# Kernel optimization log

Hardware: AMD Instinct MI355X
Metric: run time of the kernel (lower is better)

## Reference

```python
import jax, jax.numpy as jnp
import numpy as np

# model_grid_shape (flipped ensemble grid, all equal here); E = 8 experts
GRID = (2, 2, 2)
E = GRID[0] * GRID[1] * GRID[2]
N = 524288   # query points
H = 64       # sub-model MLP hidden width


def setup_inputs() -> dict:
    key = jax.random.key(0)
    ks = jax.random.split(key, 4)
    # query coordinates in [-1, 1]^3
    x = jax.random.uniform(ks[0], (N, 3), jnp.float32, -1.0, 1.0)
    # per-expert spatial extents: axis-aligned cells tiling [-1,1]^3, in the
    # same flat order as the routing index i0 + i1*g0 + i2*g0*g1
    i = np.arange(E)
    cell = np.stack([i % GRID[0], (i // GRID[0]) % GRID[1],
                     i // (GRID[0] * GRID[1])], axis=-1).astype(np.float32)
    g = np.array(GRID, np.float32)
    extents_min = jnp.asarray(-1.0 + 2.0 * cell / g)          # [E, 3]
    extents_max = jnp.asarray(-1.0 + 2.0 * (cell + 1.0) / g)  # [E, 3]
    # per-expert SRN MLP parameters: 3 -> H -> H -> 1
    W1 = jax.random.normal(ks[1], (E, 3, H), jnp.float32) / np.sqrt(3.0)
    b1 = jnp.zeros((E, H), jnp.float32)
    W2 = jax.random.normal(ks[2], (E, H, H), jnp.float32) / np.sqrt(float(H))
    b2 = jnp.zeros((E, H), jnp.float32)
    W3 = jax.random.normal(ks[3], (E, H, 1), jnp.float32) / np.sqrt(float(H))
    b3 = jnp.zeros((E, 1), jnp.float32)
    return {"x": x, "extents_min": extents_min, "extents_max": extents_max,
            "W1": W1, "b1": b1, "W2": W2, "b2": b2, "W3": W3, "b3": b3}


def reference(x, extents_min, extents_max, W1, b1, W2, b2, W3, b3):
    # --- routing: flat expert index per point (matches torch forward) ---
    u = jnp.clip((x + 1.0) * 0.5, 0.0, 0.99)
    gvec = jnp.asarray(GRID, x.dtype)
    gi = (u * gvec).astype(jnp.int32)                       # [N, 3]
    idx = gi[:, 0] + gi[:, 1] * GRID[0] + gi[:, 2] * (GRID[0] * GRID[1])

    # --- dispatch/combine: scan over experts, masked scatter into y ---
    def body(y, args):
        i, emin, emax, w1, bb1, w2, bb2, w3, bb3 = args
        # normalize point into expert-local [-1, 1]^3
        xn = -1.0 + 2.0 * ((x - emin) / (emax - emin))      # [N, 3]
        h = jax.nn.relu(xn @ w1 + bb1)                      # [N, H]
        h = jax.nn.relu(h @ w2 + bb2)                       # [N, H]
        o = h @ w3 + bb3                                    # [N, 1]
        mask = (idx == i)[:, None]
        return jnp.where(mask, o, y), None

    y0 = jnp.zeros((x.shape[0], 1), x.dtype)
    y, _ = jax.lax.scan(
        body, y0,
        (jnp.arange(E), extents_min, extents_max, W1, b1, W2, b2, W3, b3))
    return y
```

## Files before the change

### kernel.cpp

```cpp
#include <hip/hip_runtime.h>

typedef __bf16 bf16x8 __attribute__((ext_vector_type(8)));
typedef __bf16 bf16x2 __attribute__((ext_vector_type(2)));
typedef float f32x4 __attribute__((ext_vector_type(4)));
typedef float f32x2 __attribute__((ext_vector_type(2)));

#define N_PTS 524288
#define SBLK 256
#define PTS_PER_SBLK 2048
#define CAP 73728

__device__ __forceinline__ unsigned short f2bf(float f) {
    unsigned u = __float_as_uint(f);
    u += 0x7FFFu + ((u >> 16) & 1u);
    return (unsigned short)(u >> 16);
}

__device__ __forceinline__ int route(float x0, float x1, float x2) {
    int g0 = (int)(fminf(fmaxf((x0 + 1.0f) * 0.5f, 0.0f), 0.99f) * 2.0f);
    int g1 = (int)(fminf(fmaxf((x1 + 1.0f) * 0.5f, 0.0f), 0.99f) * 2.0f);
    int g2 = (int)(fminf(fmaxf((x2 + 1.0f) * 0.5f, 0.0f), 0.99f) * 2.0f);
    return g0 + 2*g1 + 4*g2;
}

#define OFF_CNT  0u
#define OFF_XG   1024u

extern "C" __global__ void __launch_bounds__(256) k3_scatter(
        const float* __restrict__ x, int* __restrict__ cursor,
        float4* __restrict__ xg) {
    __shared__ int lh[8];
    __shared__ int startS[8];
    int t = threadIdx.x;
    if (t < 8) lh[t] = 0;
    __syncthreads();
    int base = blockIdx.x * PTS_PER_SBLK;
    float c0[8], c1[8], c2[8];
    unsigned epack = 0;
    #pragma unroll
    for (int i = 0; i < 8; ++i) {
        int p = base + i * 256 + t;
        c0[i] = x[3*p]; c1[i] = x[3*p+1]; c2[i] = x[3*p+2];
        int e = route(c0[i], c1[i], c2[i]);
        epack |= (unsigned)e << (3*i);
        atomicAdd(&lh[e], 1);
    }
    __syncthreads();
    if (t < 8) { startS[t] = atomicAdd(&cursor[t], lh[t]); lh[t] = 0; }
    __syncthreads();
    #pragma unroll
    for (int i = 0; i < 8; ++i) {
        int e = (epack >> (3*i)) & 7;
        int r = atomicAdd(&lh[e], 1);
        float4 v;
        v.x = c0[i]; v.y = c1[i]; v.z = c2[i];
        v.w = __uint_as_float((unsigned)(base + i * 256 + t));
        xg[e*CAP + startS[e] + r] = v;
    }
}

extern "C" __global__ void __launch_bounds__(256, 3) k4_mlp(
        const float4* __restrict__ xg, const int* __restrict__ cursor,
        const float* __restrict__ emin, const float* __restrict__ emax,
        const float* __restrict__ W1, const float* __restrict__ b1,
        const float* __restrict__ W2, const float* __restrict__ b2,
        const float* __restrict__ W3, const float* __restrict__ b3,
        float* __restrict__ y) {
    int e = blockIdx.y;
    int cnt = cursor[e];
    int tileStart = blockIdx.x * 256;
    if (tileStart >= cnt) return;
    int base = e * CAP;

    int t = threadIdx.x;
    int lane = t & 63, wave = t >> 6;
    int m16 = lane & 15;
    int g  = lane >> 4;
    int g8 = g * 8;

    __shared__ __align__(16) unsigned short h1s[256][72];
    __shared__ __align__(16) unsigned short w2t[64][72];
    __shared__ float4 w1s[64];
    __shared__ float  b2s[64], w3s[64];

    if (t < 64) {
        int n = t;
        float d0 = emax[e*3+0] - emin[e*3+0];
        float d1 = emax[e*3+1] - emin[e*3+1];
        float d2 = emax[e*3+2] - emin[e*3+2];
        float a0 = 2.0f/d0, a1 = 2.0f/d1, a2 = 2.0f/d2;
        float cc0 = -1.0f - 2.0f*emin[e*3+0]/d0;
        float cc1 = -1.0f - 2.0f*emin[e*3+1]/d1;
        float cc2 = -1.0f - 2.0f*emin[e*3+2]/d2;
        float w0 = W1[(e*3+0)*64 + n];
        float w1 = W1[(e*3+1)*64 + n];
        float w2 = W1[(e*3+2)*64 + n];
        float4 w;
        w.x = a0*w0; w.y = a1*w1; w.z = a2*w2;
        w.w = cc0*w0 + cc1*w1 + cc2*w2 + b1[e*64 + n];
        w1s[n] = w;
    } else if (t < 128) {
        b2s[t - 64]  = b2[e*64 + (t - 64)];
    } else if (t < 192) {
        w3s[t - 128] = W3[e*64 + (t - 128)];
    }
    #pragma unroll
    for (int i = 0; i < 16; ++i) {
        int idx = i * 256 + t;
        int k = idx >> 6, n = idx & 63;
        w2t[n][k] = f2bf(W2[(e*64 + k)*64 + n]);
    }

    int valid = (tileStart + t) < cnt;
    float px = 0.f, py = 0.f, pz = 0.f;
    unsigned pidx = 0;
    if (valid) {
        float4 v = xg[base + tileStart + t];
        px = v.x; py = v.y; pz = v.z; pidx = __float_as_uint(v.w);
    }
    __syncthreads();

    #pragma unroll
    for (int jb = 0; jb < 8; ++jb) {
        bf16x8 hv;
        #pragma unroll
        for (int j2 = 0; j2 < 8; j2 += 2) {
            float4 wa = w1s[jb*8 + j2];
            float4 wb = w1s[jb*8 + j2 + 1];
            float ha = fmaf(px, wa.x, fmaf(py, wa.y, fmaf(pz, wa.z, wa.w)));
            float hb = fmaf(px, wb.x, fmaf(py, wb.y, fmaf(pz, wb.z, wb.w)));
            f32x2 hp;
            hp[0] = fmaxf(ha, 0.0f);
            hp[1] = fmaxf(hb, 0.0f);
            bf16x2 bp = __builtin_convertvector(hp, bf16x2);
            hv[j2] = bp[0]; hv[j2+1] = bp[1];
        }
        *(bf16x8*)(&h1s[t][jb*8]) = hv;
    }
    __syncthreads();

    bf16x8 A[4][2];
    #pragma unroll
    for (int mt = 0; mt < 4; ++mt)
        #pragma unroll
        for (int kt = 0; kt < 2; ++kt)
            A[mt][kt] = *(const bf16x8*)(&w2t[mt*16 + m16][kt*32 + g8]);

    f32x4 acc[4][4] = {};
    #pragma unroll
    for (int pt = 0; pt < 4; ++pt) {
        int row = wave*64 + pt*16 + m16;
        bf16x8 B0 = *(const bf16x8*)(&h1s[row][g8]);
        bf16x8 B1 = *(const bf16x8*)(&h1s[row][32 + g8]);
        #pragma unroll
        for (int mt = 0; mt < 4; ++mt) {
            acc[mt][pt] = __builtin_amdgcn_mfma_f32_16x16x32_bf16(A[mt][0], B0, acc[mt][pt], 0, 0, 0);
            acc[mt][pt] = __builtin_amdgcn_mfma_f32_16x16x32_bf16(A[mt][1], B1, acc[mt][pt], 0, 0, 0);
        }
    }

    float bb3 = b3[e];
    #pragma unroll
    for (int pt = 0; pt < 4; ++pt) {
        float s = 0.0f;
        #pragma unroll
        for (int mt = 0; mt < 4; ++mt) {
            #pragma unroll
            for (int r = 0; r < 4; ++r) {
                int f = mt*16 + g*4 + r;
                float h2 = fmaxf(acc[mt][pt][r] + b2s[f], 0.0f);
                s = fmaf(h2, w3s[f], s);
            }
        }
        s += __shfl_xor(s, 16, 64);
        s += __shfl_xor(s, 32, 64);
        unsigned oi = (unsigned)__shfl((int)pidx, pt*16 + m16, 64);
        int row = wave*64 + pt*16 + m16;
        if (lane < 16 && (tileStart + row) < cnt) {
            y[oi] = s + bb3;
        }
    }
}

extern "C" void kernel_launch(void* const* d_in, const int* in_sizes, int n_in,
                              void* d_out, int out_size, void* d_ws, size_t ws_size,
                              hipStream_t stream) {
    const float* x    = (const float*)d_in[0];
    const float* emin = (const float*)d_in[1];
    const float* emax = (const float*)d_in[2];
    const float* W1   = (const float*)d_in[3];
    const float* b1   = (const float*)d_in[4];
    const float* W2   = (const float*)d_in[5];
    const float* b2   = (const float*)d_in[6];
    const float* W3   = (const float*)d_in[7];
    const float* b3   = (const float*)d_in[8];
    float* y = (float*)d_out;

    char* ws = (char*)d_ws;
    int*  cursor = (int*)(ws + OFF_CNT);
    float4* xg   = (float4*)(ws + OFF_XG);

    hipMemsetAsync(cursor, 0, 8 * sizeof(int), stream);
    k3_scatter<<<SBLK, 256, 0, stream>>>(x, cursor, xg);
    k4_mlp<<<dim3(288, 8), 256, 0, stream>>>(xg, cursor, emin, emax,
                                             W1, b1, W2, b2, W3, b3, y);
}
```

Before: 97.33 us.

## Replace global atomic cursors with per-block histograms and in-kernel prefix scan

```diff
diff --git a/kernel.cpp b/kernel.cpp
--- a/kernel.cpp
+++ b/kernel.cpp
@@ -8,7 +8,6 @@
 #define N_PTS 524288
 #define SBLK 256
 #define PTS_PER_SBLK 2048
-#define CAP 73728
 
 __device__ __forceinline__ unsigned short f2bf(float f) {
     unsigned u = __float_as_uint(f);
@@ -23,18 +22,20 @@
     return g0 + 2*g1 + 4*g2;
 }
 
-#define OFF_CNT  0u
-#define OFF_XG   1024u
-
-extern "C" __global__ void __launch_bounds__(256) k3_scatter(
-        const float* __restrict__ x, int* __restrict__ cursor,
-        float4* __restrict__ xg) {
+#define OFF_HCNT 0u
+#define OFF_HOFF 8192u
+#define OFF_XG   16384u
+
+extern "C" __global__ void __launch_bounds__(256) k3d_scatter(
+        const float* __restrict__ x, int* __restrict__ hcntG,
+        int* __restrict__ hoffG, float4* __restrict__ xg) {
     __shared__ int lh[8];
-    __shared__ int startS[8];
+    __shared__ int loff[8];
     int t = threadIdx.x;
+    int b = blockIdx.x;
     if (t < 8) lh[t] = 0;
     __syncthreads();
-    int base = blockIdx.x * PTS_PER_SBLK;
+    int base = b * PTS_PER_SBLK;
     float c0[8], c1[8], c2[8];
     unsigned epack = 0;
     #pragma unroll
@@ -46,7 +47,17 @@
         atomicAdd(&lh[e], 1);
     }
     __syncthreads();
-    if (t < 8) { startS[t] = atomicAdd(&cursor[t], lh[t]); lh[t] = 0; }
+    if (t == 0) {
+        int run = 0;
+        #pragma unroll
+        for (int e = 0; e < 8; ++e) { loff[e] = run; run += lh[e]; }
+    }
+    __syncthreads();
+    if (t < 8) {
+        hcntG[t*256 + b] = lh[t];
+        hoffG[t*256 + b] = loff[t];
+        lh[t] = 0;
+    }
     __syncthreads();
     #pragma unroll
     for (int i = 0; i < 8; ++i) {
@@ -55,22 +66,20 @@
         float4 v;
         v.x = c0[i]; v.y = c1[i]; v.z = c2[i];
         v.w = __uint_as_float((unsigned)(base + i * 256 + t));
-        xg[e*CAP + startS[e] + r] = v;
+        xg[base + loff[e] + r] = v;
     }
 }
 
 extern "C" __global__ void __launch_bounds__(256, 3) k4_mlp(
-        const float4* __restrict__ xg, const int* __restrict__ cursor,
+        const float4* __restrict__ xg, const int* __restrict__ hcntG,
+        const int* __restrict__ hoffG,
         const float* __restrict__ emin, const float* __restrict__ emax,
         const float* __restrict__ W1, const float* __restrict__ b1,
         const float* __restrict__ W2, const float* __restrict__ b2,
         const float* __restrict__ W3, const float* __restrict__ b3,
         float* __restrict__ y) {
     int e = blockIdx.y;
-    int cnt = cursor[e];
     int tileStart = blockIdx.x * 256;
-    if (tileStart >= cnt) return;
-    int base = e * CAP;
 
     int t = threadIdx.x;
     int lane = t & 63, wave = t >> 6;
@@ -82,6 +91,11 @@
     __shared__ __align__(16) unsigned short w2t[64][72];
     __shared__ float4 w1s[64];
     __shared__ float  b2s[64], w3s[64];
+    __shared__ int hcnt[256], hoff[256], hscan[256];
+
+    hcnt[t] = hcntG[e*256 + t];
+    hoff[t] = hoffG[e*256 + t];
+    hscan[t] = hcnt[t];
 
     if (t < 64) {
         int n = t;
@@ -111,14 +125,34 @@
         w2t[n][k] = f2bf(W2[(e*64 + k)*64 + n]);
     }
 
+    int incl = hcnt[t];
+    #pragma unroll
+    for (int off = 1; off < 256; off <<= 1) {
+        __syncthreads();
+        int add = (t >= off) ? hscan[t - off] : 0;
+        __syncthreads();
+        if (t >= off) { incl += add; hscan[t] = incl; }
+    }
+    __syncthreads();
+    int cnt = hscan[255];
+    if (tileStart >= cnt) return;
+
     int valid = (tileStart + t) < cnt;
     float px = 0.f, py = 0.f, pz = 0.f;
     unsigned pidx = 0;
     if (valid) {
-        float4 v = xg[base + tileStart + t];
+        int s = tileStart + t;
+        int lo = 0, hi = 255;
+        #pragma unroll
+        for (int it = 0; it < 8; ++it) {
+            int mid = (lo + hi) >> 1;
+            if (hscan[mid] > s) hi = mid; else lo = mid + 1;
+        }
+        int bsrc = lo;
+        int local = s - (hscan[bsrc] - hcnt[bsrc]);
+        float4 v = xg[bsrc * PTS_PER_SBLK + hoff[bsrc] + local];
         px = v.x; py = v.y; pz = v.z; pidx = __float_as_uint(v.w);
     }
-    __syncthreads();
 
     #pragma unroll
     for (int jb = 0; jb < 8; ++jb) {
@@ -197,11 +231,11 @@
     float* y = (float*)d_out;
 
     char* ws = (char*)d_ws;
-    int*  cursor = (int*)(ws + OFF_CNT);
-    float4* xg   = (float4*)(ws + OFF_XG);
-
-    hipMemsetAsync(cursor, 0, 8 * sizeof(int), stream);
-    k3_scatter<<<SBLK, 256, 0, stream>>>(x, cursor, xg);
-    k4_mlp<<<dim3(288, 8), 256, 0, stream>>>(xg, cursor, emin, emax,
+    int* hcntG  = (int*)(ws + OFF_HCNT);
+    int* hoffG  = (int*)(ws + OFF_HOFF);
+    float4* xg  = (float4*)(ws + OFF_XG);
+
+    k3d_scatter<<<SBLK, 256, 0, stream>>>(x, hcntG, hoffG, xg);
+    k4_mlp<<<dim3(288, 8), 256, 0, stream>>>(xg, hcntG, hoffG, emin, emax,
                                              W1, b1, W2, b2, W3, b3, y);
 }
```

After: 98.67 us. About the same (+1.4%).
